# Performance work log

Hardware: AMD Instinct MI355X
Metric: run time of the kernel (lower is better)

The kernel has to match this reference:

```python
import jax, jax.numpy as jnp
import numpy as np

# Config (lite version of KimiK2): 2 layers, dim 2048, 16 heads x 128, MLA latent rank 512,
# 4 experts / top-2, SwiGLU inter dim 1024, vocab 32000, batch 2, seq 1024.
DEPTH, DIM, H, HD, R, DFF, E, TOPK, V, B, S = 2, 2048, 16, 128, 512, 1024, 4, 2, 32000, 2, 1024
EPS = 1e-6


def rmsnorm(x, w):
    var = jnp.mean(jnp.square(x), axis=-1, keepdims=True)
    return x * jax.lax.rsqrt(var + EPS) * w


def setup_inputs() -> dict:
    key = jax.random.key(0)
    ks = jax.random.split(key, 16)
    sd = 0.02
    d = {
        'x_tokens': jax.random.randint(ks[0], (B, S), 0, V),
        'emb': jax.random.normal(ks[1], (V, DIM), jnp.float32) * sd,
        'embed_norm_w': jnp.ones((DIM,), jnp.float32),
        # per-layer stacked params (leading axis DEPTH)
        'norm_w': jnp.ones((DEPTH, DIM), jnp.float32),
        'Wq': jax.random.normal(ks[2], (DEPTH, DIM, H * HD), jnp.float32) * sd,
        'Wdkv': jax.random.normal(ks[3], (DEPTH, DIM, R), jnp.float32) * sd,
        'Wuk': jax.random.normal(ks[4], (DEPTH, R, H * HD), jnp.float32) * sd,
        'Wuv': jax.random.normal(ks[5], (DEPTH, R, H * HD), jnp.float32) * sd,
        'Wo': jax.random.normal(ks[6], (DEPTH, H * HD, DIM), jnp.float32) * sd,
        'Wg': jax.random.normal(ks[7], (DEPTH, DIM, E), jnp.float32) * sd,
        'W1': jax.random.normal(ks[8], (DEPTH, E, DIM, DFF), jnp.float32) * sd,
        'W3': jax.random.normal(ks[9], (DEPTH, E, DIM, DFF), jnp.float32) * sd,
        'W2': jax.random.normal(ks[10], (DEPTH, E, DFF, DIM), jnp.float32) * sd,
        'head_norm_w': jnp.ones((DIM,), jnp.float32),
        'head_W': jax.random.normal(ks[11], (DIM, V), jnp.float32) * sd,
        'head_b': jnp.zeros((V,), jnp.float32),
    }
    return d


def mla(x, Wq, Wdkv, Wuk, Wuv, Wo):
    # Multi-head latent attention: queries from x, K/V from a low-rank latent c.
    Bq, Sq, _ = x.shape
    q = (x @ Wq).reshape(Bq, Sq, H, HD)
    c = x @ Wdkv                                   # [B,S,R] compressed KV latent
    k = (c @ Wuk).reshape(Bq, Sq, H, HD)
    v = (c @ Wuv).reshape(Bq, Sq, H, HD)
    scores = jnp.einsum('bqhd,bkhd->bhqk', q, k) / jnp.sqrt(jnp.float32(HD))
    a = jax.nn.softmax(scores, axis=-1)            # block never passes a mask -> full attention
    o = jnp.einsum('bhqk,bkhd->bqhd', a, v).reshape(Bq, Sq, H * HD)
    return o @ Wo


def moe(x, Wg, W1, W3, W2):
    # x: [B,S,D] -> flatten tokens. Dense-over-experts (E=4) with top-k masked gates.
    Bq, Sq, Dq = x.shape
    xt = x.reshape(Bq * Sq, Dq)                    # [T,D]
    gate = jax.nn.softmax(xt @ Wg, axis=-1)        # [T,E]
    topv, topi = jax.lax.top_k(gate, TOPK)
    topv = topv / jnp.sum(topv, axis=-1, keepdims=True)
    gw = jnp.zeros_like(gate).at[jnp.arange(xt.shape[0])[:, None], topi].set(topv)  # [T,E]
    h = jnp.einsum('td,edf->etf', xt, W1)
    g = jnp.einsum('td,edf->etf', xt, W3)
    eo = jnp.einsum('etf,efd->etd', jax.nn.silu(h) * g, W2)
    out = jnp.einsum('etd,te->td', eo, gw)
    return out.reshape(Bq, Sq, Dq)


def reference(x_tokens, emb, embed_norm_w, norm_w, Wq, Wdkv, Wuk, Wuv, Wo, Wg, W1, W3, W2, head_norm_w, head_W, head_b):
    h = emb[x_tokens]
    h = rmsnorm(h, embed_norm_w)

    def layer(h, p):
        nw, wq, wdkv, wuk, wuv, wo, wg, w1, w3, w2 = p
        h = h + mla(rmsnorm(h, nw), wq, wdkv, wuk, wuv, wo)
        # NOTE: same norm weight reused pre-MoE, as in the torch module
        h = h + moe(rmsnorm(h, nw), wg, w1, w3, w2)
        return h, None

    h, _ = jax.lax.scan(layer, h, (norm_w, Wq, Wdkv, Wuk, Wuv, Wo, Wg, W1, W3, W2))
    return rmsnorm(h, head_norm_w) @ head_W + head_b
```

## Files before the change

### kernel.cpp

```cpp
#include <hip/hip_runtime.h>
#include <hip/hip_bf16.h>

typedef __hip_bfloat16 bf16;
typedef __bf16 bf16x8 __attribute__((ext_vector_type(8)));
typedef float f32x4 __attribute__((ext_vector_type(4)));
typedef unsigned short u16;
typedef unsigned int u32;
typedef __attribute__((address_space(1))) const void* gptr_t;
typedef __attribute__((address_space(3))) void* lptr_t;

static constexpr int TOKS = 2048, DM = 2048, RL = 512, DF = 1024, SQ = 1024, NV = 32000;
static constexpr long PL_X  = (long)TOKS * DM;
static constexpr long PL_C  = (long)TOKS * RL;
static constexpr long PL_VT = 2l * 16 * 128 * 1024;
static constexpr long M4 = 4l * 1024 * 1024;
static constexpr long M2 = 2l * 1024 * 1024;

__device__ __forceinline__ float b2f(bf16 x){ return __bfloat162float(x); }
__device__ __forceinline__ bf16  f2b(float x){ return __float2bfloat16(x); }
__device__ __forceinline__ void split1(float x, u16& h, u16& l){
  bf16 hb = f2b(x);
  float r = x - b2f(hb);
  bf16 lb = f2b(r);
  h = *(u16*)&hb; l = *(u16*)&lb;
}

__device__ __forceinline__ float block_red(float v, int op){
  __shared__ float red[4];
  const int lane = threadIdx.x & 63, wv = threadIdx.x >> 6;
  #pragma unroll
  for (int off = 32; off > 0; off >>= 1){
    float o = __shfl_down(v, off, 64);
    v = op ? fmaxf(v, o) : v + o;
  }
  __syncthreads();
  if (lane == 0) red[wv] = v;
  __syncthreads();
  float r = red[0];
  #pragma unroll
  for (int i = 1; i < 4; ++i) r = op ? fmaxf(r, red[i]) : r + red[i];
  return r;
}

__global__ __launch_bounds__(256)
void embed_norm_k(const int* __restrict__ toks, const float* __restrict__ emb,
                  const float* __restrict__ w, float* __restrict__ h){
  const int t = blockIdx.x;
  const long tok = toks[t];
  const int base = threadIdx.x * 8;
  const float* ep = emb + tok * (long)DM + base;
  float4 va = *(const float4*)ep, vb = *(const float4*)(ep + 4);
  float v[8] = {va.x, va.y, va.z, va.w, vb.x, vb.y, vb.z, vb.w};
  float ss = 0.f;
  #pragma unroll
  for (int i = 0; i < 8; ++i) ss += v[i]*v[i];
  ss = block_red(ss, 0);
  const float inv = rsqrtf(ss / DM + 1e-6f);
  float4 wa = *(const float4*)(w + base), wb4 = *(const float4*)(w + base + 4);
  float wv[8] = {wa.x, wa.y, wa.z, wa.w, wb4.x, wb4.y, wb4.z, wb4.w};
  float* hp = h + (long)t * DM + base;
  #pragma unroll
  for (int i = 0; i < 8; ++i) hp[i] = v[i] * inv * wv[i];
}

__global__ __launch_bounds__(256)
void rmsnorm_planes_k(const float* __restrict__ h, const float* __restrict__ w,
                      u16* __restrict__ hi, u16* __restrict__ lo){
  const int t = blockIdx.x;
  const int base = threadIdx.x * 8;
  const float* hp = h + (long)t * DM + base;
  float4 va = *(const float4*)hp, vb = *(const float4*)(hp + 4);
  float v[8] = {va.x, va.y, va.z, va.w, vb.x, vb.y, vb.z, vb.w};
  float ss = 0.f;
  #pragma unroll
  for (int i = 0; i < 8; ++i) ss += v[i]*v[i];
  ss = block_red(ss, 0);
  const float inv = rsqrtf(ss / DM + 1e-6f);
  float4 wa = *(const float4*)(w + base), wb4 = *(const float4*)(w + base + 4);
  float wv[8] = {wa.x, wa.y, wa.z, wa.w, wb4.x, wb4.y, wb4.z, wb4.w};
  u16 hvv[8], lvv[8];
  #pragma unroll
  for (int i = 0; i < 8; ++i) split1(v[i] * inv * wv[i], hvv[i], lvv[i]);
  *(int4*)(hi + (long)t * DM + base) = *(const int4*)hvv;
  *(int4*)(lo + (long)t * DM + base) = *(const int4*)lvv;
}

__global__ __launch_bounds__(256)
void gate_k(const float* __restrict__ h, const float* __restrict__ nw,
            const float* __restrict__ Wg, float* __restrict__ gw){
  const int t = blockIdx.x;
  const int base = threadIdx.x * 8;
  const float* hp = h + (long)t * DM + base;
  float4 va = *(const float4*)hp, vb = *(const float4*)(hp + 4);
  float v[8] = {va.x, va.y, va.z, va.w, vb.x, vb.y, vb.z, vb.w};
  float ss = 0.f;
  #pragma unroll
  for (int i = 0; i < 8; ++i) ss += v[i]*v[i];
  ss = block_red(ss, 0);
  const float inv = rsqrtf(ss / DM + 1e-6f);
  float a[4] = {0.f, 0.f, 0.f, 0.f};
  #pragma unroll
  for (int i = 0; i < 8; ++i){
    const float xv = v[i] * inv * nw[base + i];
    #pragma unroll
    for (int e = 0; e < 4; ++e) a[e] += xv * Wg[(base + i)*4 + e];
  }
  #pragma unroll
  for (int e = 0; e < 4; ++e) a[e] = block_red(a[e], 0);
  if (threadIdx.x == 0){
    int i1 = 0;
    for (int e = 1; e < 4; ++e) if (a[e] > a[i1]) i1 = e;
    int i2 = -1;
    for (int e = 0; e < 4; ++e){ if (e == i1) continue; if (i2 < 0 || a[e] > a[i2]) i2 = e; }
    float g[4];
    const float m = fmaxf(fmaxf(a[0], a[1]), fmaxf(a[2], a[3]));
    float s = 0.f;
    for (int e = 0; e < 4; ++e){ g[e] = __expf(a[e] - m); s += g[e]; }
    for (int e = 0; e < 4; ++e) g[e] /= s;
    const float ns = g[i1] + g[i2];
    float* op = gw + (long)t * 4;
    op[0] = 0.f; op[1] = 0.f; op[2] = 0.f; op[3] = 0.f;
    op[i1] = g[i1] / ns; op[i2] = g[i2] / ns;
  }
}

__global__ __launch_bounds__(256)
void softmax_pack_k(float* __restrict__ pf){
  const long row = blockIdx.x;
  const float* pr = pf + row * SQ;
  const int base = threadIdx.x * 4;
  float4 v4 = *(const float4*)(pr + base);
  float v[4] = {v4.x, v4.y, v4.z, v4.w};
  float m = fmaxf(fmaxf(v[0], v[1]), fmaxf(v[2], v[3]));
  m = block_red(m, 1);
  float s = 0.f;
  #pragma unroll
  for (int i = 0; i < 4; ++i){ v[i] = __expf(v[i] - m); s += v[i]; }
  s = block_red(s, 0);
  const float inv = 1.f / s;
  u16 hv[4], lv[4];
  #pragma unroll
  for (int i = 0; i < 4; ++i) split1(v[i] * inv, hv[i], lv[i]);
  u16* out = (u16*)pf + row * 2048;
  *(int2*)(out + base) = *(const int2*)hv;
  *(int2*)(out + 1024 + base) = *(const int2*)lv;
}

__global__ __launch_bounds__(256)
void swiglu_pack_k(float* __restrict__ h1, const float* __restrict__ h3){
  const int t = threadIdx.x;
  const long r = (long)blockIdx.x * 2 + (t >> 7);
  const int col = (t & 127) * 8;
  const float* p1 = h1 + r * 1024 + col;
  const float* p3 = h3 + r * 1024 + col;
  float4 a0 = *(const float4*)p1, a1 = *(const float4*)(p1 + 4);
  float4 b0 = *(const float4*)p3, b1 = *(const float4*)(p3 + 4);
  float a[8] = {a0.x, a0.y, a0.z, a0.w, a1.x, a1.y, a1.z, a1.w};
  float b[8] = {b0.x, b0.y, b0.z, b0.w, b1.x, b1.y, b1.z, b1.w};
  u16 hv[8], lv[8];
  #pragma unroll
  for (int j = 0; j < 8; ++j){
    const float y = (a[j] / (1.f + __expf(-a[j]))) * b[j];
    split1(y, hv[j], lv[j]);
  }
  __syncthreads();
  u16* out = (u16*)h1 + r * 2048;
  *(int4*)(out + col) = *(const int4*)hv;
  *(int4*)(out + 1024 + col) = *(const int4*)lv;
}

__global__ __launch_bounds__(256)
void swiglu_bk(bf16* __restrict__ h1, const bf16* __restrict__ h3){
  const long i = ((long)blockIdx.x * 256 + threadIdx.x) * 8;
  union { int4 i4; bf16 b[8]; } x, y;
  x.i4 = *(const int4*)(h1 + i);
  y.i4 = *(const int4*)(h3 + i);
  #pragma unroll
  for (int j = 0; j < 8; ++j){
    const float a = b2f(x.b[j]);
    const float b = b2f(y.b[j]);
    x.b[j] = f2b((a / (1.f + __expf(-a))) * b);
  }
  *(int4*)(h1 + i) = x.i4;
}

__global__ __launch_bounds__(256)
void tsplit_k(const float* __restrict__ in, long inz, int ldin,
              u16* __restrict__ oh, u16* __restrict__ ol, long outz, int ldout, int ntx){
  __shared__ u16 lh[64][72], ll[64][72];
  const int z = blockIdx.z;
  in += (long)z * inz; oh += (long)z * outz; ol += (long)z * outz;
  const int bx = blockIdx.x % ntx, by = blockIdx.x / ntx;
  const int k0 = by * 64, n0 = bx * 64;
  const int t = threadIdx.x;
  {
    const int r = t >> 2, cb = (t & 3) * 16;
    const float* ip = in + (long)(k0 + r) * ldin + n0 + cb;
    #pragma unroll
    for (int i = 0; i < 16; i += 4){
      float4 v = *(const float4*)(ip + i);
      float a[4] = {v.x, v.y, v.z, v.w};
      #pragma unroll
      for (int j = 0; j < 4; ++j){
        u16 hv, lv; split1(a[j], hv, lv);
        lh[r][cb + i + j] = hv; ll[r][cb + i + j] = lv;
      }
    }
  }
  __syncthreads();
  {
    const int n = t >> 2, kb = (t & 3) * 16;
    u16 hv[16], lv[16];
    #pragma unroll
    for (int i = 0; i < 16; ++i){ hv[i] = lh[kb + i][n]; lv[i] = ll[kb + i][n]; }
    u16* po = oh + (long)(n0 + n) * ldout + k0 + kb;
    u16* pl = ol + (long)(n0 + n) * ldout + k0 + kb;
    *(int4*)po = *(const int4*)hv; *(int4*)(po + 8) = *(const int4*)(hv + 8);
    *(int4*)pl = *(const int4*)lv; *(int4*)(pl + 8) = *(const int4*)(lv + 8);
  }
}

__global__ __launch_bounds__(256)
void tconv_k(const float* __restrict__ in, long inz, int ldin,
             bf16* __restrict__ out, long outz, int ldout, int ntx){
  __shared__ u16 lh[64][72];
  const int z = blockIdx.z;
  in += (long)z * inz; out += (long)z * outz;
  const int bx = blockIdx.x % ntx, by = blockIdx.x / ntx;
  const int k0 = by * 64, n0 = bx * 64;
  const int t = threadIdx.x;
  {
    const int r = t >> 2, cb = (t & 3) * 16;
    const float* ip = in + (long)(k0 + r) * ldin + n0 + cb;
    #pragma unroll
    for (int i = 0; i < 16; i += 4){
      float4 v = *(const float4*)(ip + i);
      float a[4] = {v.x, v.y, v.z, v.w};
      #pragma unroll
      for (int j = 0; j < 4; ++j){ bf16 hb = f2b(a[j]); lh[r][cb + i + j] = *(u16*)&hb; }
    }
  }
  __syncthreads();
  {
    const int n = t >> 2, kb = (t & 3) * 16;
    u16 hv[16];
    #pragma unroll
    for (int i = 0; i < 16; ++i) hv[i] = lh[kb + i][n];
    u16* po = (u16*)out + (long)(n0 + n) * ldout + k0 + kb;
    *(int4*)po = *(const int4*)hv; *(int4*)(po + 8) = *(const int4*)(hv + 8);
  }
}

__device__ __forceinline__ int swz2(int r, int c){
  return ((((c >> 3) + (r >> 1)) & 3) << 3) | (c & 7);
}
__device__ __forceinline__ int2 tile_xy(int ny){
  const int nwg = gridDim.x;
  const int wid = blockIdx.x;
  const int q = nwg >> 3, r = nwg & 7;
  const int xcd = wid & 7, pos = wid >> 3;
  const int lid = (xcd < r) ? (xcd*(q+1) + pos) : (r*(q+1) + (xcd - r)*q + pos);
  return make_int2(lid / ny, lid % ny);
}

__device__ __forceinline__ void stage_issue(const u16* src, int ld, int rbase, int k0,
                                            u16* lp, int sub, int lane){
  const int r = sub * 16 + (lane >> 2);
  const int cs = ((lane & 3) - (r >> 1)) & 3;
  const u16* g = src + (long)(rbase + r) * ld + k0 + cs * 8;
  __builtin_amdgcn_global_load_lds((gptr_t)g, (lptr_t)(lp + sub * 512), 16, 0, 0);
}

template<int MT, int OM>
__global__ __launch_bounds__(256)
void gemms_nt(const u16* __restrict__ Ah, const u16* __restrict__ Al, long ab, int lda,
              const u16* __restrict__ Bh, const u16* __restrict__ Bl, long bb, int ldb,
              void* __restrict__ Cv, long cb, int ldc, long cpl,
              int K, float scale, const float* __restrict__ aux, int gst, int ny)
{
  __shared__ __align__(16) u16 ash[MT*32][32], asl[MT*32][32];
  __shared__ __align__(16) u16 bsh[128][32], bsl[128][32];
  const int z = blockIdx.z;
  Ah += (long)z * ab; Al += (long)z * ab;
  Bh += (long)z * bb; Bl += (long)z * bb;
  const int2 tt = tile_xy(ny);
  const int m0 = tt.y * (MT*32), n0 = tt.x * 128;
  const int tid = threadIdx.x, lane = tid & 63, wv = tid >> 6;
  const int wr = (wv >> 1) * (MT*16), wc = (wv & 1) * 64;
  const int fr = lane & 15, fk = (lane >> 4) * 8;

  f32x4 acc[MT][4] = {};
  constexpr int AI = MT * 2;

  for (int k0 = 0; k0 < K; k0 += 32){
    __syncthreads();
    #pragma unroll
    for (int ii = 0; ii < 2*AI + 16; ++ii){
      if ((ii & 3) != wv) continue;
      if (ii < AI)            stage_issue(Ah, lda, m0, k0, &ash[0][0], ii, lane);
      else if (ii < 2*AI)     stage_issue(Al, lda, m0, k0, &asl[0][0], ii - AI, lane);
      else if (ii < 2*AI + 8) stage_issue(Bh, ldb, n0, k0, &bsh[0][0], ii - 2*AI, lane);
      else                    stage_issue(Bl, ldb, n0, k0, &bsl[0][0], ii - 2*AI - 8, lane);
    }
    __syncthreads();
    bf16x8 ahf[MT], alf[MT], bhf[4], blf[4];
    #pragma unroll
    for (int mi = 0; mi < MT; ++mi){
      const int rr = wr + mi * 16 + fr;
      const int sc = swz2(rr, fk);
      ahf[mi] = *(const bf16x8*)&ash[rr][sc];
      alf[mi] = *(const bf16x8*)&asl[rr][sc];
    }
    #pragma unroll
    for (int ni = 0; ni < 4; ++ni){
      const int rr = wc + ni * 16 + fr;
      const int sc = swz2(rr, fk);
      bhf[ni] = *(const bf16x8*)&bsh[rr][sc];
      blf[ni] = *(const bf16x8*)&bsl[rr][sc];
    }
    #pragma unroll
    for (int mi = 0; mi < MT; ++mi)
      #pragma unroll
      for (int ni = 0; ni < 4; ++ni){
        acc[mi][ni] = __builtin_amdgcn_mfma_f32_16x16x32_bf16(ahf[mi], bhf[ni], acc[mi][ni], 0, 0, 0);
        acc[mi][ni] = __builtin_amdgcn_mfma_f32_16x16x32_bf16(ahf[mi], blf[ni], acc[mi][ni], 0, 0, 0);
        acc[mi][ni] = __builtin_amdgcn_mfma_f32_16x16x32_bf16(alf[mi], bhf[ni], acc[mi][ni], 0, 0, 0);
      }
  }

  const int crow = (lane >> 4) * 4, ccol = lane & 15;
  #pragma unroll
  for (int mi = 0; mi < MT; ++mi){
    #pragma unroll
    for (int ni = 0; ni < 4; ++ni){
      const int gm0 = m0 + wr + mi * 16 + crow;
      const int gn = n0 + wc + ni * 16 + ccol;
      if (OM == 5){
        u16 hv[4], lv[4];
        #pragma unroll
        for (int j = 0; j < 4; ++j) split1(acc[mi][ni][j], hv[j], lv[j]);
        const long off = (((long)(gm0 >> 10) * 16 + (gn >> 7)) * 128 + (gn & 127)) * 1024 + (gm0 & 1023);
        u16* vt = (u16*)Cv;
        *(int2*)(vt + off) = *(const int2*)hv;
        *(int2*)(vt + cpl + off) = *(const int2*)lv;
      } else {
        #pragma unroll
        for (int j = 0; j < 4; ++j){
          const long off = (long)z * cb + (long)(gm0 + j) * ldc + gn;
          const float v = acc[mi][ni][j];
          if (OM == 0)      ((float*)Cv)[off] = v * scale;
          else if (OM == 1) ((float*)Cv)[off] += v;
          else if (OM == 3) ((float*)Cv)[off] += aux[(long)(gm0 + j) * gst] * v;
          else { u16 hv, lv; split1(v, hv, lv); ((u16*)Cv)[off] = hv; ((u16*)Cv)[off + cpl] = lv; }
        }
      }
    }
  }
}

template<int MT, int OM>
__global__ __launch_bounds__(256)
void gemmb_nt(const bf16* __restrict__ A, long ab, int lda,
              const bf16* __restrict__ B, long bb, int ldb,
              void* __restrict__ Cv, long cb, int ldc,
              int K, const float* __restrict__ aux, int gst, int ny)
{
  __shared__ __align__(16) u16 a_lds[MT*32][32];
  __shared__ __align__(16) u16 b_lds[128][32];
  const int z = blockIdx.z;
  A += (long)z * ab; B += (long)z * bb;
  const int2 tt = tile_xy(ny);
  const int m0 = tt.y * (MT*32), n0 = tt.x * 128;
  const int tid = threadIdx.x, lane = tid & 63, wv = tid >> 6;
  const int wr = (wv >> 1) * (MT*16), wc = (wv & 1) * 64;
  const int fr = lane & 15, fk = (lane >> 4) * 8;

  f32x4 acc[MT][4] = {};
  constexpr int AI = MT * 2;

  for (int k0 = 0; k0 < K; k0 += 32){
    __syncthreads();
    #pragma unroll
    for (int ii = 0; ii < AI + 8; ++ii){
      if ((ii & 3) != wv) continue;
      if (ii < AI) stage_issue((const u16*)A, lda, m0, k0, &a_lds[0][0], ii, lane);
      else         stage_issue((const u16*)B, ldb, n0, k0, &b_lds[0][0], ii - AI, lane);
    }
    __syncthreads();
    bf16x8 af[MT], bfv[4];
    #pragma unroll
    for (int mi = 0; mi < MT; ++mi){
      const int rr = wr + mi * 16 + fr;
      af[mi] = *(const bf16x8*)&a_lds[rr][swz2(rr, fk)];
    }
    #pragma unroll
    for (int ni = 0; ni < 4; ++ni){
      const int rr = wc + ni * 16 + fr;
      bfv[ni] = *(const bf16x8*)&b_lds[rr][swz2(rr, fk)];
    }
    #pragma unroll
    for (int mi = 0; mi < MT; ++mi)
      #pragma unroll
      for (int ni = 0; ni < 4; ++ni)
        acc[mi][ni] = __builtin_amdgcn_mfma_f32_16x16x32_bf16(af[mi], bfv[ni], acc[mi][ni], 0, 0, 0);
  }

  const int crow = (lane >> 4) * 4, ccol = lane & 15;
  #pragma unroll
  for (int mi = 0; mi < MT; ++mi){
    #pragma unroll
    for (int ni = 0; ni < 4; ++ni){
      const int gm0 = m0 + wr + mi * 16 + crow;
      const int gn = n0 + wc + ni * 16 + ccol;
      #pragma unroll
      for (int j = 0; j < 4; ++j){
        const long off = (long)z * cb + (long)(gm0 + j) * ldc + gn;
        const float v = acc[mi][ni][j];
        if (OM == 0)      ((bf16*)Cv)[off] = f2b(v);
        else if (OM == 2) ((float*)Cv)[off] = v + aux[gn];
        else              atomicAdd(&((float*)Cv)[off], aux[(long)(gm0 + j) * gst + z] * v);
      }
    }
  }
}

extern "C" void kernel_launch(void* const* d_in, const int* in_sizes, int n_in,
                              void* d_out, int out_size, void* d_ws, size_t ws_size,
                              hipStream_t stream)
{
  (void)in_sizes; (void)n_in; (void)out_size; (void)ws_size;
  const int*   toks = (const int*)d_in[0];
  const float* emb  = (const float*)d_in[1];
  const float* enw  = (const float*)d_in[2];
  const float* nw   = (const float*)d_in[3];
  const float* Wq   = (const float*)d_in[4];
  const float* Wdkv = (const float*)d_in[5];
  const float* Wuk  = (const float*)d_in[6];
  const float* Wuv  = (const float*)d_in[7];
  const float* Wo   = (const float*)d_in[8];
  const float* Wg   = (const float*)d_in[9];
  const float* W1   = (const float*)d_in[10];
  const float* W3   = (const float*)d_in[11];
  const float* W2   = (const float*)d_in[12];
  const float* hnw  = (const float*)d_in[13];
  const float* hW   = (const float*)d_in[14];
  const float* hb   = (const float*)d_in[15];

  const size_t MB = 1ull << 20;
  char* ws = (char*)d_ws;
  float* h    = (float*)(ws);
  float* gw   = (float*)(ws + 16*MB);
  u16*   xph  = (u16*)(ws + 17*MB);
  u16*   wpl  = (u16*)(ws + 33*MB);
  u16*   qph  = (u16*)(ws + 49*MB);
  u16*   cph  = (u16*)(ws + 65*MB);
  u16*   kph  = (u16*)(ws + 69*MB);
  u16*   vtp  = (u16*)(ws + 85*MB);
  u16*   oph  = (u16*)(ws + 101*MB);
  float* pf   = (float*)(ws + 17*MB);
  float* h1f  = (float*)(ws + 49*MB);
  float* h3f  = (float*)(ws + 65*MB);
  bf16*  wT   = (bf16*)(ws + 33*MB);
  bf16*  h1b  = (bf16*)(ws + 49*MB);
  bf16*  h3b  = (bf16*)(ws + 65*MB);
  bf16*  whT  = (bf16*)(ws + 33*MB);

  const float qscale = 0.08838834764831845f;

  embed_norm_k<<<TOKS, 256, 0, stream>>>(toks, emb, enw, h);

  for (int l = 0; l < 2; ++l){
    const float* nwl = nw + (long)l * DM;
    rmsnorm_planes_k<<<TOKS, 256, 0, stream>>>(h, nwl, xph, xph + PL_X);

    tsplit_k<<<1024, 256, 0, stream>>>(Wq + (long)l*DM*DM, 0, DM, wpl, wpl + M4, 0, DM, 32);
    gemms_nt<2,4><<<dim3(512,1,1), 256, 0, stream>>>(xph, xph + PL_X, 0, DM, wpl, wpl + M4, 0, DM,
        qph, 0, DM, PL_X, DM, 1.f, nullptr, 0, 32);
    tsplit_k<<<256, 256, 0, stream>>>(Wdkv + (long)l*DM*RL, 0, RL, wpl, wpl + M2, 0, DM, 8);
    gemms_nt<2,4><<<dim3(128,1,1), 256, 0, stream>>>(xph, xph + PL_X, 0, DM, wpl, wpl + M2, 0, DM,
        cph, 0, RL, PL_C, DM, 1.f, nullptr, 0, 32);
    tsplit_k<<<256, 256, 0, stream>>>(Wuk + (long)l*RL*DM, 0, DM, wpl, wpl + M2, 0, RL, 32);
    gemms_nt<2,4><<<dim3(512,1,1), 256, 0, stream>>>(cph, cph + PL_C, 0, RL, wpl, wpl + M2, 0, RL,
        kph, 0, DM, PL_X, RL, 1.f, nullptr, 0, 32);
    tsplit_k<<<256, 256, 0, stream>>>(Wuv + (long)l*RL*DM, 0, DM, wpl, wpl + M2, 0, RL, 32);
    gemms_nt<2,5><<<dim3(512,1,1), 256, 0, stream>>>(cph, cph + PL_C, 0, RL, wpl, wpl + M2, 0, RL,
        vtp, 0, 0, PL_VT, RL, 1.f, nullptr, 0, 32);

    for (int b = 0; b < 2; ++b){
      for (int hg = 0; hg < 2; ++hg){
        const long qo = (long)b*SQ*DM + hg*1024;
        gemms_nt<4,0><<<dim3(64,1,8), 256, 0, stream>>>(qph + qo, qph + PL_X + qo, 128, DM,
            kph + qo, kph + PL_X + qo, 128, DM,
            pf, (long)SQ*SQ, SQ, 0, 128, qscale, nullptr, 0, 8);
        softmax_pack_k<<<8*SQ, 256, 0, stream>>>(pf);
        const long vo = ((long)b*16 + hg*8) * 128 * 1024;
        gemms_nt<1,4><<<dim3(32,1,8), 256, 0, stream>>>((const u16*)pf, (const u16*)pf + 1024,
            1024l*2048, 2048,
            vtp + vo, vtp + PL_VT + vo, 128l*1024, 1024,
            oph + (long)b*SQ*DM + hg*1024, 128, DM, PL_X, SQ, 1.f, nullptr, 0, 32);
      }
    }

    tsplit_k<<<1024, 256, 0, stream>>>(Wo + (long)l*DM*DM, 0, DM, wpl, wpl + M4, 0, DM, 32);
    gemms_nt<2,1><<<dim3(512,1,1), 256, 0, stream>>>(oph, oph + PL_X, 0, DM, wpl, wpl + M4, 0, DM,
        h, 0, DM, 0, DM, 1.f, nullptr, 0, 32);

    gate_k<<<TOKS, 256, 0, stream>>>(h, nwl, Wg + (long)l*DM*4, gw);
    rmsnorm_planes_k<<<TOKS, 256, 0, stream>>>(h, nwl, xph, xph + PL_X);

    if (l == 0){
      for (int p2 = 0; p2 < 2; ++p2){
        const long wo13 = ((long)l*4 + p2*2) * (long)DM * DF;
        tsplit_k<<<dim3(512,1,2), 256, 0, stream>>>(W1 + wo13, (long)DM*DF, DF, wpl, wpl + M4, M2, DM, 16);
        gemms_nt<2,0><<<dim3(256,1,2), 256, 0, stream>>>(xph, xph + PL_X, 0, DM, wpl, wpl + M4, M2, DM,
            h1f, (long)TOKS*DF, DF, 0, DM, 1.f, nullptr, 0, 32);
        tsplit_k<<<dim3(512,1,2), 256, 0, stream>>>(W3 + wo13, (long)DM*DF, DF, wpl, wpl + M4, M2, DM, 16);
        gemms_nt<2,0><<<dim3(256,1,2), 256, 0, stream>>>(xph, xph + PL_X, 0, DM, wpl, wpl + M4, M2, DM,
            h3f, (long)TOKS*DF, DF, 0, DM, 1.f, nullptr, 0, 32);
        swiglu_pack_k<<<2048, 256, 0, stream>>>(h1f, h3f);
        tsplit_k<<<dim3(512,1,2), 256, 0, stream>>>(W2 + ((long)l*4 + p2*2)*(long)DF*DM, (long)DF*DM, DM,
            wpl, wpl + M4, M2, DF, 32);
        for (int ei = 0; ei < 2; ++ei){
          gemms_nt<2,3><<<dim3(512,1,1), 256, 0, stream>>>(
              (const u16*)h1f + (long)ei*TOKS*2048, (const u16*)h1f + (long)ei*TOKS*2048 + 1024,
              0, 2048, wpl + (long)ei*M2, wpl + M4 + (long)ei*M2, 0, DF,
              h, 0, DM, 0, DF, 1.f, gw + p2*2 + ei, 4, 32);
        }
      }
    } else {
      tconv_k<<<dim3(512,1,4), 256, 0, stream>>>(W1 + (long)l*4*DM*DF, (long)DM*DF, DF, wT, M2, DM, 16);
      gemmb_nt<2,0><<<dim3(256,1,4), 256, 0, stream>>>((const bf16*)xph, 0, DM, wT, M2, DM,
          h1b, (long)TOKS*DF, DF, DM, nullptr, 0, 32);
      tconv_k<<<dim3(512,1,4), 256, 0, stream>>>(W3 + (long)l*4*DM*DF, (long)DM*DF, DF, wT, M2, DM, 16);
      gemmb_nt<2,0><<<dim3(256,1,4), 256, 0, stream>>>((const bf16*)xph, 0, DM, wT, M2, DM,
          h3b, (long)TOKS*DF, DF, DM, nullptr, 0, 32);
      swiglu_bk<<<4096, 256, 0, stream>>>(h1b, h3b);
      tconv_k<<<dim3(512,1,4), 256, 0, stream>>>(W2 + (long)l*4*DF*DM, (long)DF*DM, DM, wT, M2, DF, 32);
      gemmb_nt<4,3><<<dim3(256,1,4), 256, 0, stream>>>(h1b, (long)TOKS*DF, DF, wT, M2, DF,
          h, 0, DM, DF, gw, 4, 16);
    }
  }

  rmsnorm_planes_k<<<TOKS, 256, 0, stream>>>(h, hnw, xph, xph + PL_X);
  for (int half = 0; half < 2; ++half){
    tconv_k<<<8000, 256, 0, stream>>>(hW + half*16000, 0, NV, whT, 0, DM, 250);
    gemmb_nt<4,2><<<dim3(2000,1,1), 256, 0, stream>>>((const bf16*)xph, 0, DM, whT, 0, DM,
        (float*)d_out + half*16000, 0, NV, DM, hb + half*16000, 0, 16);
  }
}
```

Baseline: 2.300 ms.

## Dispatch MoE tokens sparsely per expert with capacity-bounded gather and scatter

Builds per-expert token lists from the top-2 gate weights using a ballot/popcount kernel, gathers only the routed token rows, and runs the expert up/gate/down GEMMs on those compacted rows. GEMM tiles past the expert's token count exit early. The down-projection epilogue scatters the weighted results back to the original token rows. This removes the dense compute over all tokens for every expert, whose results were mostly multiplied by zero gate weights. In exchange it adds gather kernels and an indexed, atomic epilogue, and it imposes a fixed per-expert capacity of 1536 that would silently drop tokens if routing were very unbalanced.

Measured after the change: 2.291 ms. No clear change (-0.4%).

```diff
diff --git a/kernel.cpp b/kernel.cpp
--- a/kernel.cpp
+++ b/kernel.cpp
@@ -10,6 +10,7 @@
 typedef __attribute__((address_space(3))) void* lptr_t;
 
 static constexpr int TOKS = 2048, DM = 2048, RL = 512, DF = 1024, SQ = 1024, NV = 32000;
+static constexpr int CAP = 1536;
 static constexpr long PL_X  = (long)TOKS * DM;
 static constexpr long PL_C  = (long)TOKS * RL;
 static constexpr long PL_VT = 2l * 16 * 128 * 1024;
@@ -125,6 +126,43 @@
 }
 
 __global__ __launch_bounds__(256)
+void build_lists_k(const float* __restrict__ gw, int* __restrict__ idx, int* __restrict__ cnt){
+  const int e = threadIdx.x >> 6, lane = threadIdx.x & 63;
+  int base = 0;
+  for (int t0 = 0; t0 < TOKS; t0 += 64){
+    const int t = t0 + lane;
+    const bool sel = gw[(long)t * 4 + e] > 0.f;
+    const unsigned long long m = __ballot(sel);
+    const int pos = __popcll(m & ((1ull << lane) - 1ull));
+    if (sel && base + pos < CAP) idx[e * CAP + base + pos] = t;
+    base += (int)__popcll(m);
+  }
+  if (lane == 0) cnt[e] = base < CAP ? base : CAP;
+}
+
+__global__ __launch_bounds__(256)
+void gather2_k(const u16* __restrict__ xph, const int* __restrict__ idx,
+               const int* __restrict__ cnt, int ebase, u16* __restrict__ xg){
+  const int e = blockIdx.x / CAP, r = blockIdx.x % CAP;
+  if (r >= cnt[ebase + e]) return;
+  const long t = idx[(long)(ebase + e) * CAP + r];
+  const int c = threadIdx.x * 8;
+  const long dst = ((long)e * 2 * CAP + r) * DM + c;
+  *(int4*)(xg + dst) = *(const int4*)(xph + t * DM + c);
+  *(int4*)(xg + dst + (long)CAP * DM) = *(const int4*)(xph + PL_X + t * DM + c);
+}
+
+__global__ __launch_bounds__(256)
+void gatherb_k(const u16* __restrict__ xph, const int* __restrict__ idx,
+               const int* __restrict__ cnt, u16* __restrict__ xgb){
+  const int e = blockIdx.x / CAP, r = blockIdx.x % CAP;
+  if (r >= cnt[e]) return;
+  const long t = idx[(long)e * CAP + r];
+  const int c = threadIdx.x * 8;
+  *(int4*)(xgb + ((long)e * CAP + r) * DM + c) = *(const int4*)(xph + t * DM + c);
+}
+
+__global__ __launch_bounds__(256)
 void softmax_pack_k(float* __restrict__ pf){
   const long row = blockIdx.x;
   const float* pr = pf + row * SQ;
@@ -276,7 +314,8 @@
 void gemms_nt(const u16* __restrict__ Ah, const u16* __restrict__ Al, long ab, int lda,
               const u16* __restrict__ Bh, const u16* __restrict__ Bl, long bb, int ldb,
               void* __restrict__ Cv, long cb, int ldc, long cpl,
-              int K, float scale, const float* __restrict__ aux, int gst, int ny)
+              int K, float scale, const float* __restrict__ aux, int gst, int ny,
+              const int* __restrict__ rowmap, const int* __restrict__ cntp)
 {
   __shared__ __align__(16) u16 ash[MT*32][32], asl[MT*32][32];
   __shared__ __align__(16) u16 bsh[128][32], bsl[128][32];
@@ -285,6 +324,8 @@
   Bh += (long)z * bb; Bl += (long)z * bb;
   const int2 tt = tile_xy(ny);
   const int m0 = tt.y * (MT*32), n0 = tt.x * 128;
+  int cntv = 1 << 30;
+  if (cntp){ cntv = cntp[z]; if (m0 >= cntv) return; }
   const int tid = threadIdx.x, lane = tid & 63, wv = tid >> 6;
   const int wr = (wv >> 1) * (MT*16), wc = (wv & 1) * 64;
   const int fr = lane & 15, fk = (lane >> 4) * 8;
@@ -343,6 +384,15 @@
         u16* vt = (u16*)Cv;
         *(int2*)(vt + off) = *(const int2*)hv;
         *(int2*)(vt + cpl + off) = *(const int2*)lv;
+      } else if (OM == 6){
+        #pragma unroll
+        for (int j = 0; j < 4; ++j){
+          const int row = gm0 + j;
+          if (row < cntv){
+            const long t = rowmap[(long)z * CAP + row];
+            ((float*)Cv)[t * ldc + gn] += aux[t * gst] * acc[mi][ni][j];
+          }
+        }
       } else {
         #pragma unroll
         for (int j = 0; j < 4; ++j){
@@ -363,7 +413,8 @@
 void gemmb_nt(const bf16* __restrict__ A, long ab, int lda,
               const bf16* __restrict__ B, long bb, int ldb,
               void* __restrict__ Cv, long cb, int ldc,
-              int K, const float* __restrict__ aux, int gst, int ny)
+              int K, const float* __restrict__ aux, int gst, int ny,
+              const int* __restrict__ rowmap, const int* __restrict__ cntp)
 {
   __shared__ __align__(16) u16 a_lds[MT*32][32];
   __shared__ __align__(16) u16 b_lds[128][32];
@@ -371,6 +422,8 @@
   A += (long)z * ab; B += (long)z * bb;
   const int2 tt = tile_xy(ny);
   const int m0 = tt.y * (MT*32), n0 = tt.x * 128;
+  int cntv = 1 << 30;
+  if (cntp){ cntv = cntp[z]; if (m0 >= cntv) return; }
   const int tid = threadIdx.x, lane = tid & 63, wv = tid >> 6;
   const int wr = (wv >> 1) * (MT*16), wc = (wv & 1) * 64;
   const int fr = lane & 15, fk = (lane >> 4) * 8;
@@ -414,11 +467,19 @@
       const int gn = n0 + wc + ni * 16 + ccol;
       #pragma unroll
       for (int j = 0; j < 4; ++j){
-        const long off = (long)z * cb + (long)(gm0 + j) * ldc + gn;
         const float v = acc[mi][ni][j];
-        if (OM == 0)      ((bf16*)Cv)[off] = f2b(v);
-        else if (OM == 2) ((float*)Cv)[off] = v + aux[gn];
-        else              atomicAdd(&((float*)Cv)[off], aux[(long)(gm0 + j) * gst + z] * v);
+        if (OM == 7){
+          const int row = gm0 + j;
+          if (row < cntv){
+            const long t = rowmap[(long)z * CAP + row];
+            atomicAdd(&((float*)Cv)[t * ldc + gn], aux[t * gst + z] * v);
+          }
+        } else {
+          const long off = (long)z * cb + (long)(gm0 + j) * ldc + gn;
+          if (OM == 0)      ((bf16*)Cv)[off] = f2b(v);
+          else if (OM == 2) ((float*)Cv)[off] = v + aux[gn];
+          else              atomicAdd(&((float*)Cv)[off], aux[(long)(gm0 + j) * gst + z] * v);
+        }
       }
     }
   }
@@ -450,6 +511,8 @@
   char* ws = (char*)d_ws;
   float* h    = (float*)(ws);
   float* gw   = (float*)(ws + 16*MB);
+  int*   idx  = (int*)(ws + 16*MB + 128*1024);
+  int*   cnt  = (int*)(ws + 16*MB + 256*1024);
   u16*   xph  = (u16*)(ws + 17*MB);
   u16*   wpl  = (u16*)(ws + 33*MB);
   u16*   qph  = (u16*)(ws + 49*MB);
@@ -458,11 +521,13 @@
   u16*   vtp  = (u16*)(ws + 85*MB);
   u16*   oph  = (u16*)(ws + 101*MB);
   float* pf   = (float*)(ws + 17*MB);
-  float* h1f  = (float*)(ws + 49*MB);
-  float* h3f  = (float*)(ws + 65*MB);
+  u16*   xg   = (u16*)(ws + 49*MB);
+  float* h1f  = (float*)(ws + 73*MB);
+  float* h3f  = (float*)(ws + 85*MB);
   bf16*  wT   = (bf16*)(ws + 33*MB);
-  bf16*  h1b  = (bf16*)(ws + 49*MB);
-  bf16*  h3b  = (bf16*)(ws + 65*MB);
+  u16*   xgb  = (u16*)(ws + 49*MB);
+  bf16*  h1b  = (bf16*)(ws + 73*MB);
+  bf16*  h3b  = (bf16*)(ws + 85*MB);
   bf16*  whT  = (bf16*)(ws + 33*MB);
 
   const float qscale = 0.08838834764831845f;
@@ -475,69 +540,76 @@
 
     tsplit_k<<<1024, 256, 0, stream>>>(Wq + (long)l*DM*DM, 0, DM, wpl, wpl + M4, 0, DM, 32);
     gemms_nt<2,4><<<dim3(512,1,1), 256, 0, stream>>>(xph, xph + PL_X, 0, DM, wpl, wpl + M4, 0, DM,
-        qph, 0, DM, PL_X, DM, 1.f, nullptr, 0, 32);
+        qph, 0, DM, PL_X, DM, 1.f, nullptr, 0, 32, nullptr, nullptr);
     tsplit_k<<<256, 256, 0, stream>>>(Wdkv + (long)l*DM*RL, 0, RL, wpl, wpl + M2, 0, DM, 8);
     gemms_nt<2,4><<<dim3(128,1,1), 256, 0, stream>>>(xph, xph + PL_X, 0, DM, wpl, wpl + M2, 0, DM,
-        cph, 0, RL, PL_C, DM, 1.f, nullptr, 0, 32);
+        cph, 0, RL, PL_C, DM, 1.f, nullptr, 0, 32, nullptr, nullptr);
     tsplit_k<<<256, 256, 0, stream>>>(Wuk + (long)l*RL*DM, 0, DM, wpl, wpl + M2, 0, RL, 32);
     gemms_nt<2,4><<<dim3(512,1,1), 256, 0, stream>>>(cph, cph + PL_C, 0, RL, wpl, wpl + M2, 0, RL,
-        kph, 0, DM, PL_X, RL, 1.f, nullptr, 0, 32);
+        kph, 0, DM, PL_X, RL, 1.f, nullptr, 0, 32, nullptr, nullptr);
     tsplit_k<<<256, 256, 0, stream>>>(Wuv + (long)l*RL*DM, 0, DM, wpl, wpl + M2, 0, RL, 32);
     gemms_nt<2,5><<<dim3(512,1,1), 256, 0, stream>>>(cph, cph + PL_C, 0, RL, wpl, wpl + M2, 0, RL,
-        vtp, 0, 0, PL_VT, RL, 1.f, nullptr, 0, 32);
+        vtp, 0, 0, PL_VT, RL, 1.f, nullptr, 0, 32, nullptr, nullptr);
 
     for (int b = 0; b < 2; ++b){
       for (int hg = 0; hg < 2; ++hg){
         const long qo = (long)b*SQ*DM + hg*1024;
         gemms_nt<4,0><<<dim3(64,1,8), 256, 0, stream>>>(qph + qo, qph + PL_X + qo, 128, DM,
             kph + qo, kph + PL_X + qo, 128, DM,
-            pf, (long)SQ*SQ, SQ, 0, 128, qscale, nullptr, 0, 8);
+            pf, (long)SQ*SQ, SQ, 0, 128, qscale, nullptr, 0, 8, nullptr, nullptr);
         softmax_pack_k<<<8*SQ, 256, 0, stream>>>(pf);
         const long vo = ((long)b*16 + hg*8) * 128 * 1024;
         gemms_nt<1,4><<<dim3(32,1,8), 256, 0, stream>>>((const u16*)pf, (const u16*)pf + 1024,
             1024l*2048, 2048,
             vtp + vo, vtp + PL_VT + vo, 128l*1024, 1024,
-            oph + (long)b*SQ*DM + hg*1024, 128, DM, PL_X, SQ, 1.f, nullptr, 0, 32);
+            oph + (long)b*SQ*DM + hg*1024, 128, DM, PL_X, SQ, 1.f, nullptr, 0, 32, nullptr, nullptr);
       }
     }
 
     tsplit_k<<<1024, 256, 0, stream>>>(Wo + (long)l*DM*DM, 0, DM, wpl, wpl + M4, 0, DM, 32);
     gemms_nt<2,1><<<dim3(512,1,1), 256, 0, stream>>>(oph, oph + PL_X, 0, DM, wpl, wpl + M4, 0, DM,
-        h, 0, DM, 0, DM, 1.f, nullptr, 0, 32);
+        h, 0, DM, 0, DM, 1.f, nullptr, 0, 32, nullptr, nullptr);
 
     gate_k<<<TOKS, 256, 0, stream>>>(h, nwl, Wg + (long)l*DM*4, gw);
+    build_lists_k<<<1, 256, 0, stream>>>(gw, idx, cnt);
     rmsnorm_planes_k<<<TOKS, 256, 0, stream>>>(h, nwl, xph, xph + PL_X);
 
     if (l == 0){
       for (int p2 = 0; p2 < 2; ++p2){
-        const long wo13 = ((long)l*4 + p2*2) * (long)DM * DF;
+        const int ebase = p2 * 2;
+        const long wo13 = ((long)l*4 + ebase) * (long)DM * DF;
+        gather2_k<<<2*CAP, 256, 0, stream>>>(xph, idx, cnt, ebase, xg);
         tsplit_k<<<dim3(512,1,2), 256, 0, stream>>>(W1 + wo13, (long)DM*DF, DF, wpl, wpl + M4, M2, DM, 16);
-        gemms_nt<2,0><<<dim3(256,1,2), 256, 0, stream>>>(xph, xph + PL_X, 0, DM, wpl, wpl + M4, M2, DM,
-            h1f, (long)TOKS*DF, DF, 0, DM, 1.f, nullptr, 0, 32);
+        gemms_nt<2,0><<<dim3(192,1,2), 256, 0, stream>>>(xg, xg + (long)CAP*DM, 2l*CAP*DM, DM,
+            wpl, wpl + M4, M2, DM, h1f, (long)CAP*DF, DF, 0, DM, 1.f, nullptr, 0, 24,
+            nullptr, cnt + ebase);
         tsplit_k<<<dim3(512,1,2), 256, 0, stream>>>(W3 + wo13, (long)DM*DF, DF, wpl, wpl + M4, M2, DM, 16);
-        gemms_nt<2,0><<<dim3(256,1,2), 256, 0, stream>>>(xph, xph + PL_X, 0, DM, wpl, wpl + M4, M2, DM,
-            h3f, (long)TOKS*DF, DF, 0, DM, 1.f, nullptr, 0, 32);
-        swiglu_pack_k<<<2048, 256, 0, stream>>>(h1f, h3f);
-        tsplit_k<<<dim3(512,1,2), 256, 0, stream>>>(W2 + ((long)l*4 + p2*2)*(long)DF*DM, (long)DF*DM, DM,
+        gemms_nt<2,0><<<dim3(192,1,2), 256, 0, stream>>>(xg, xg + (long)CAP*DM, 2l*CAP*DM, DM,
+            wpl, wpl + M4, M2, DM, h3f, (long)CAP*DF, DF, 0, DM, 1.f, nullptr, 0, 24,
+            nullptr, cnt + ebase);
+        swiglu_pack_k<<<CAP, 256, 0, stream>>>(h1f, h3f);
+        tsplit_k<<<dim3(512,1,2), 256, 0, stream>>>(W2 + ((long)l*4 + ebase)*(long)DF*DM, (long)DF*DM, DM,
             wpl, wpl + M4, M2, DF, 32);
         for (int ei = 0; ei < 2; ++ei){
-          gemms_nt<2,3><<<dim3(512,1,1), 256, 0, stream>>>(
-              (const u16*)h1f + (long)ei*TOKS*2048, (const u16*)h1f + (long)ei*TOKS*2048 + 1024,
+          gemms_nt<2,6><<<dim3(384,1,1), 256, 0, stream>>>(
+              (const u16*)h1f + (long)ei*CAP*2048, (const u16*)h1f + (long)ei*CAP*2048 + 1024,
               0, 2048, wpl + (long)ei*M2, wpl + M4 + (long)ei*M2, 0, DF,
-              h, 0, DM, 0, DF, 1.f, gw + p2*2 + ei, 4, 32);
+              h, 0, DM, 0, DF, 1.f, gw + ebase + ei, 4, 24,
+              idx + (ebase + ei)*CAP, cnt + ebase + ei);
         }
       }
     } else {
+      gatherb_k<<<4*CAP, 256, 0, stream>>>(xph, idx, cnt, xgb);
       tconv_k<<<dim3(512,1,4), 256, 0, stream>>>(W1 + (long)l*4*DM*DF, (long)DM*DF, DF, wT, M2, DM, 16);
-      gemmb_nt<2,0><<<dim3(256,1,4), 256, 0, stream>>>((const bf16*)xph, 0, DM, wT, M2, DM,
-          h1b, (long)TOKS*DF, DF, DM, nullptr, 0, 32);
+      gemmb_nt<2,0><<<dim3(192,1,4), 256, 0, stream>>>((const bf16*)xgb, (long)CAP*DM, DM, wT, M2, DM,
+          h1b, (long)CAP*DF, DF, DM, nullptr, 0, 24, nullptr, cnt);
       tconv_k<<<dim3(512,1,4), 256, 0, stream>>>(W3 + (long)l*4*DM*DF, (long)DM*DF, DF, wT, M2, DM, 16);
-      gemmb_nt<2,0><<<dim3(256,1,4), 256, 0, stream>>>((const bf16*)xph, 0, DM, wT, M2, DM,
-          h3b, (long)TOKS*DF, DF, DM, nullptr, 0, 32);
-      swiglu_bk<<<4096, 256, 0, stream>>>(h1b, h3b);
+      gemmb_nt<2,0><<<dim3(192,1,4), 256, 0, stream>>>((const bf16*)xgb, (long)CAP*DM, DM, wT, M2, DM,
+          h3b, (long)CAP*DF, DF, DM, nullptr, 0, 24, nullptr, cnt);
+      swiglu_bk<<<(4*CAP*DF)/2048, 256, 0, stream>>>(h1b, h3b);
       tconv_k<<<dim3(512,1,4), 256, 0, stream>>>(W2 + (long)l*4*DF*DM, (long)DF*DM, DM, wT, M2, DF, 32);
-      gemmb_nt<4,3><<<dim3(256,1,4), 256, 0, stream>>>(h1b, (long)TOKS*DF, DF, wT, M2, DF,
-          h, 0, DM, DF, gw, 4, 16);
+      gemmb_nt<2,7><<<dim3(384,1,4), 256, 0, stream>>>(h1b, (long)CAP*DF, DF, wT, M2, DF,
+          h, 0, DM, DF, gw, 4, 24, idx, cnt);
     }
   }
 
@@ -545,6 +617,6 @@
   for (int half = 0; half < 2; ++half){
     tconv_k<<<8000, 256, 0, stream>>>(hW + half*16000, 0, NV, whT, 0, DM, 250);
     gemmb_nt<4,2><<<dim3(2000,1,1), 256, 0, stream>>>((const bf16*)xph, 0, DM, whT, 0, DM,
-        (float*)d_out + half*16000, 0, NV, DM, hb + half*16000, 0, 16);
-  }
-}
+        (float*)d_out + half*16000, 0, NV, DM, hb + half*16000, 0, 16, nullptr, nullptr);
+  }
+}
```
